# Optimization experiments

Hardware: AMD Instinct MI355X
Metric: run time of the kernel (lower is better)

The kernel has to match this reference:

```python
import jax, jax.numpy as jnp
import numpy as np

B, N, P, L = 32, 4096, 256, 16
DR = 128           # rel_dim = args.rgcn_hidden_size
H = 128            # rnn_hidden_size (unidirectional -> rnn_opt_dim == H)
D = H
NUM_REL = 400      # num_rels * 2


def setup_inputs() -> dict:
    key = jax.random.key(0)
    ks = jax.random.split(key, 12)
    s = 0.05
    graph_embed = jax.random.normal(ks[0], (B, N, DR), jnp.float32)
    node_opt = jax.random.normal(ks[1], (B, D), jnp.float32)
    node_idx = jax.random.randint(ks[2], (B, P, L), 0, N)
    rel_idx = jax.random.randint(ks[3], (B, P, L), 0, NUM_REL)
    path_lens = jax.random.randint(ks[4], (B, P), 1, L + 1)  # in [1, L]
    rel_embeds = jax.random.normal(ks[5], (NUM_REL, DR), jnp.float32) * s
    W_ih = jax.random.normal(ks[6], (4 * H, 2 * DR), jnp.float32) * s
    W_hh = jax.random.normal(ks[7], (4 * H, H), jnp.float32) * s
    b_ih = jnp.zeros((4 * H,), jnp.float32)
    b_hh = jnp.zeros((4 * H,), jnp.float32)
    in_proj_w = jax.random.normal(ks[8], (3 * D, D), jnp.float32) * s
    in_proj_b = jnp.zeros((3 * D,), jnp.float32)
    out_proj_w = jax.random.normal(ks[9], (D, D), jnp.float32) * s
    out_proj_b = jnp.zeros((D,), jnp.float32)
    return dict(graph_embed=graph_embed, node_opt=node_opt, rel_embeds=rel_embeds,
                W_ih=W_ih, W_hh=W_hh, b_ih=b_ih, b_hh=b_hh,
                in_proj_w=in_proj_w, in_proj_b=in_proj_b,
                out_proj_w=out_proj_w, out_proj_b=out_proj_b,
                node_idx=node_idx, rel_idx=rel_idx, path_lens=path_lens)


def _forward(graph_embed, node_opt, rel_embeds, W_ih, W_hh, b_ih, b_hh,
             in_proj_w, in_proj_b, out_proj_w, out_proj_b,
             node_idx, rel_idx, path_lens):
    b, n, dr = graph_embed.shape
    p, l = node_idx.shape[1], node_idx.shape[2]
    h = W_hh.shape[1]
    dt = graph_embed.dtype

    t = jnp.arange(l)
    # node embedding valid for steps < len; rel valid for steps < len-1 ('Padr' at last step -> zero rel half)
    node_mask = (t[None, None, :] < path_lens[:, :, None]).astype(dt)[..., None]
    rel_mask = (t[None, None, :] < (path_lens - 1)[:, :, None]).astype(dt)[..., None]

    batch_ix = jnp.arange(b)[:, None, None]
    node_e = graph_embed[batch_ix, node_idx]            # [B,P,L,DR]
    rel_e = rel_embeds[rel_idx]                          # [B,P,L,DR]
    x = jnp.concatenate([node_e * node_mask, rel_e * rel_mask], axis=-1)
    x = x.reshape(b * p, l, 2 * dr)                      # packed path sequences

    bias = b_ih + b_hh

    def step(carry, xt):
        hh, cc = carry
        g = xt @ W_ih.T + hh @ W_hh.T + bias
        i, f, gg, o = jnp.split(g, 4, axis=-1)
        i = jax.nn.sigmoid(i); f = jax.nn.sigmoid(f)
        gg = jnp.tanh(gg); o = jax.nn.sigmoid(o)
        cc = f * cc + i * gg
        hh = o * jnp.tanh(cc)
        return (hh, cc), hh

    h0 = jnp.zeros((b * p, h), dt)
    _, ys = jax.lax.scan(step, (h0, h0), jnp.swapaxes(x, 0, 1))
    ys = jnp.swapaxes(ys, 0, 1).reshape(b, p, l, h)

    # last valid LSTM output per path (== pack_padded_sequence semantics, unidirectional)
    idx = jnp.broadcast_to((path_lens - 1)[:, :, None, None], (b, p, 1, h))
    last = jnp.take_along_axis(ys, idx, axis=2).squeeze(2)   # [B,P,H]

    # single-head MultiheadAttention: query = node_opt, keys/values = path encodings
    Wq, Wk, Wv = jnp.split(in_proj_w, 3, axis=0)
    bq, bk, bv = jnp.split(in_proj_b, 3)
    q = node_opt @ Wq.T + bq                                  # [B,D]
    k = last @ Wk.T + bk                                      # [B,P,D]
    v = last @ Wv.T + bv
    scale = 1.0 / jnp.sqrt(jnp.asarray(q.shape[-1], dt))
    attn = jax.nn.softmax(jnp.einsum('bd,bpd->bp', q, k) * scale, axis=-1)
    ctx = jnp.einsum('bp,bpd->bd', attn, v)
    return ctx @ out_proj_w.T + out_proj_b                    # [B,D]


def reference(graph_embed, node_opt, rel_embeds, W_ih, W_hh, b_ih, b_hh,
              in_proj_w, in_proj_b, out_proj_w, out_proj_b,
              node_idx, rel_idx, path_lens):
    return _forward(graph_embed, node_opt, rel_embeds, W_ih, W_hh, b_ih, b_hh,
                    in_proj_w, in_proj_b, out_proj_w, out_proj_b,
                    node_idx, rel_idx, path_lens)
```

## Files before the change

kernel.cpp:

```cpp
#include <hip/hip_runtime.h>
#include <hip/hip_bf16.h>


#define B_    32
#define N_    4096
#define L_    16
#define DR_   128
#define H_    128
#define G4_   512
#define AST2  264
#define NPATH 8192
#define NPB   32

typedef unsigned short bfraw;
typedef short short8 __attribute__((ext_vector_type(8)));
typedef float f32x4 __attribute__((ext_vector_type(4)));

__device__ int   g_isbf16;
__device__ int   g_isi64;
__device__ __align__(16) bfraw g_Wcat[G4_ * 256];
__device__ float g_relproj[400 * G4_];
__device__ float g_bias[G4_];
__device__ int   g_perm[NPATH];
__device__ float g_last[NPATH * H_];

__device__ __forceinline__ float bfc(bfraw v) {
    return __uint_as_float(((unsigned)v) << 16);
}
__device__ __forceinline__ bfraw f2b(float f) {
    unsigned u = __float_as_uint(f);
    return (bfraw)((u + 0x7FFFu + ((u >> 16) & 1u)) >> 16);
}
__device__ __forceinline__ unsigned pk2(float a, float b) {
    return (unsigned)f2b(a) | ((unsigned)f2b(b) << 16);
}
__device__ __forceinline__ float ld(const void* p, size_t i, int isbf) {
    return isbf ? bfc(((const bfraw*)p)[i]) : ((const float*)p)[i];
}
__device__ __forceinline__ float sigf(float x) { return 1.0f / (1.0f + __expf(-x)); }
__device__ __forceinline__ float tanhfast(float x) { return 2.0f * sigf(2.0f * x) - 1.0f; }

__device__ __forceinline__ float dot128(const float* __restrict__ w,
                                        const float* __restrict__ s) {
    float acc = 0.f;
    #pragma unroll
    for (int i = 0; i < 32; ++i) {
        const float4 wv = *(const float4*)(w + i * 4);
        acc = fmaf(wv.x, s[i*4+0], fmaf(wv.y, s[i*4+1],
              fmaf(wv.z, s[i*4+2], fmaf(wv.w, s[i*4+3], acc))));
    }
    return acc;
}

__global__ __launch_bounds__(512) void k_prep(
    const void* __restrict__ node_opt, const int* __restrict__ node_idx,
    const void* __restrict__ rel_embeds,
    const void* __restrict__ W_ih, const void* __restrict__ W_hh,
    const void* __restrict__ b_ih, const void* __restrict__ b_hh,
    const int* __restrict__ path_lens)
{
    __shared__ float relv[DR_];
    __shared__ int s_big, s_nz, hist[16], cur[16];
    const int tid = threadIdx.x;
    const int blk = blockIdx.x;

    if (tid == 0) { s_big = 0; s_nz = 0; }
    __syncthreads();
    {
        const unsigned short* u = (const unsigned short*)node_opt;
        int big = 0;
        #pragma unroll
        for (int i = 0; i < 4; ++i) {
            const float v = fabsf(bfc(u[tid + i * 512]));
            big |= !(v < 1.0e3f);
        }
        if (big) s_big = 1;
        if (node_idx[2 * tid + 1] != 0) s_nz = 1;
    }
    __syncthreads();
    const int isbf = s_big ? 0 : 1;
    const int i64  = s_nz ? 0 : 1;

    if (blk < 400) {
        const int r = blk;
        if (tid < DR_) relv[tid] = ld(rel_embeds, (size_t)r * DR_ + tid, isbf);
        __syncthreads();
        const int n = tid;
        float s;
        if (isbf) {
            s = 0.f;
            for (int d = 0; d < DR_; ++d)
                s = fmaf(relv[d], bfc(((const bfraw*)W_ih)[(size_t)n * 256 + 128 + d]), s);
        } else {
            s = dot128((const float*)W_ih + (size_t)n * 256 + 128, relv);
        }
        g_relproj[r * G4_ + n] = s;
    } else if (blk < 656) {
        const int idx = (blk - 400) * 512 + tid;
        const int n = idx >> 8, k = idx & 255;
        const float v = (k < H_) ? ld(W_hh, (size_t)n * H_ + k, isbf)
                                 : ld(W_ih, (size_t)n * 256 + (k - H_), isbf);
        g_Wcat[n * 256 + k] = f2b(v);
    } else {
        if (tid == 0) { g_isbf16 = isbf; g_isi64 = i64; }
        g_bias[tid] = ld(b_ih, tid, isbf) + ld(b_hh, tid, isbf);
        if (tid < 16) hist[tid] = 0;
        __syncthreads();
        for (int p = tid; p < NPATH; p += 512) {
            const int len = i64 ? path_lens[2 * p] : path_lens[p];
            atomicAdd(&hist[len - 1], 1);
        }
        __syncthreads();
        if (tid == 0) {
            int off = 0;
            for (int b = 15; b >= 0; --b) { cur[b] = off; off += hist[b]; }
        }
        __syncthreads();
        for (int p = tid; p < NPATH; p += 512) {
            const int len = i64 ? path_lens[2 * p] : path_lens[p];
            const int pos = atomicAdd(&cur[len - 1], 1);
            g_perm[pos] = p;
        }
    }
}

__global__ __launch_bounds__(512, 2) void k_lstm(
    const void* __restrict__ graph_embed,
    const int*  __restrict__ node_idx,
    const int*  __restrict__ rel_idx,
    const int*  __restrict__ path_lens)
{
    __shared__ __align__(16) bfraw A[NPB][AST2];
    __shared__ int s_pid[NPB], s_len[NPB];
    __shared__ int s_nid[NPB][L_], s_rid[NPB][L_];

    const int isbf = g_isbf16;
    const int i64  = g_isi64;
    const int tid  = threadIdx.x;

    if (tid < NPB) {
        const int pid = g_perm[blockIdx.x * NPB + tid];
        s_pid[tid] = pid;
        s_len[tid] = i64 ? path_lens[2 * pid] : path_lens[pid];
    }
    __syncthreads();
    {
        const int m = tid >> 4, t = tid & 15;
        const int idx = s_pid[m] * L_ + t;
        s_nid[m][t] = i64 ? node_idx[2 * idx] : node_idx[idx];
        s_rid[m][t] = i64 ? rel_idx[2 * idx]  : rel_idx[idx];
    }
    {
        const int m = tid >> 4, i0 = (tid & 15) * 8;
        *(uint4*)&A[m][i0] = make_uint4(0, 0, 0, 0);
    }
    __syncthreads();

    int maxlen = 0;
    #pragma unroll
    for (int m = 0; m < NPB; ++m) maxlen = max(maxlen, s_len[m]);

    const int w    = tid >> 6;
    const int l    = tid & 63;
    const int quad = l >> 4;
    const int col  = l & 15;
    const int u0   = w * 16 + col;

    short8 wreg[8][4];
    float bq4[4];
    #pragma unroll
    for (int g = 0; g < 4; ++g) {
        bq4[g] = g_bias[g * 128 + u0];
        const bfraw* wrow = g_Wcat + (size_t)(g * 128 + u0) * 256 + quad * 8;
        #pragma unroll
        for (int ck = 0; ck < 8; ++ck)
            wreg[ck][g] = *(const short8*)(wrow + ck * 32);
    }

    const int pm  = tid >> 4;
    const int pi0 = (tid & 15) * 8;
    const size_t gbase = (size_t)(s_pid[pm] >> 8) * (size_t)(N_ * DR_);
    uint4 pn0, pn1;
    {
        const int nid = s_nid[pm][0];
        if (isbf) {
            pn0 = *(const uint4*)((const bfraw*)graph_embed + gbase + (size_t)nid * DR_ + pi0);
        } else {
            const float* gp = (const float*)graph_embed + gbase + (size_t)nid * DR_ + pi0;
            pn0 = *(const uint4*)gp; pn1 = *(const uint4*)(gp + 4);
        }
    }

    float c[2][4];
    #pragma unroll
    for (int mt = 0; mt < 2; ++mt)
        #pragma unroll
        for (int r = 0; r < 4; ++r) c[mt][r] = 0.f;

    for (int t = 0; t < maxlen; ++t) {
        {
            uint4 npk = make_uint4(0, 0, 0, 0);
            if (t < s_len[pm]) {
                if (isbf) npk = pn0;
                else {
                    const float* a = (const float*)&pn0;
                    const float* b = (const float*)&pn1;
                    npk = make_uint4(pk2(a[0],a[1]), pk2(a[2],a[3]),
                                     pk2(b[0],b[1]), pk2(b[2],b[3]));
                }
            }
            *(uint4*)&A[pm][128 + pi0] = npk;
        }
        __syncthreads();

        if (t + 1 < maxlen) {
            const int nid = s_nid[pm][t + 1];
            if (isbf) {
                pn0 = *(const uint4*)((const bfraw*)graph_embed + gbase + (size_t)nid * DR_ + pi0);
            } else {
                const float* gp = (const float*)graph_embed + gbase + (size_t)nid * DR_ + pi0;
                pn0 = *(const uint4*)gp; pn1 = *(const uint4*)(gp + 4);
            }
        }

        f32x4 acc[2][4];
        #pragma unroll
        for (int mt = 0; mt < 2; ++mt)
            #pragma unroll
            for (int g = 0; g < 4; ++g) {
                const float b = bq4[g];
                acc[mt][g][0] = b; acc[mt][g][1] = b;
                acc[mt][g][2] = b; acc[mt][g][3] = b;
            }
        #pragma unroll
        for (int ck = 0; ck < 8; ++ck) {
            const short8 a0 = *(const short8*)&A[col][ck * 32 + quad * 8];
            const short8 a1 = *(const short8*)&A[16 + col][ck * 32 + quad * 8];
            #pragma unroll
            for (int g = 0; g < 4; ++g) {
                acc[0][g] = __builtin_amdgcn_mfma_f32_16x16x32_bf16(a0, wreg[ck][g], acc[0][g], 0, 0, 0);
                acc[1][g] = __builtin_amdgcn_mfma_f32_16x16x32_bf16(a1, wreg[ck][g], acc[1][g], 0, 0, 0);
            }
        }

        float rl[2][4][4];
        #pragma unroll
        for (int mt = 0; mt < 2; ++mt)
            #pragma unroll
            for (int r = 0; r < 4; ++r) {
                const int m = mt * 16 + quad * 4 + r;
                const float* rp = g_relproj + (size_t)s_rid[m][t] * G4_ + u0;
                #pragma unroll
                for (int g = 0; g < 4; ++g) rl[mt][g][r] = rp[g * 128];
            }
        __syncthreads();

        #pragma unroll
        for (int mt = 0; mt < 2; ++mt)
            #pragma unroll
            for (int r = 0; r < 4; ++r) {
                const int m = mt * 16 + quad * 4 + r;
                const float relm = (t < s_len[m] - 1) ? 1.0f : 0.0f;
                const float ig = sigf(acc[mt][0][r] + relm * rl[mt][0][r]);
                const float fg = sigf(acc[mt][1][r] + relm * rl[mt][1][r]);
                const float gg = tanhfast(acc[mt][2][r] + relm * rl[mt][2][r]);
                const float og = sigf(acc[mt][3][r] + relm * rl[mt][3][r]);
                const float cc = fg * c[mt][r] + ig * gg;
                c[mt][r] = cc;
                const float h = og * tanhfast(cc);
                A[m][u0] = f2b(h);
                if (t == s_len[m] - 1)
                    g_last[(size_t)s_pid[m] * H_ + u0] = h;
            }
    }
}

__global__ __launch_bounds__(256) void k_attn(
    const void* __restrict__ node_opt,
    const void* __restrict__ in_proj_w,
    const void* __restrict__ in_proj_b,
    const void* __restrict__ out_proj_w,
    const void* __restrict__ out_proj_b,
    float* __restrict__ out)
{
    const int isbf = g_isbf16;
    const int b = blockIdx.x, tid = threadIdx.x;
    __shared__ __align__(16) float s_no[128], q[128], qk[128], sv2[2][128], ctx[128];
    __shared__ float logits[256];
    __shared__ float red[12];

    if (tid < 128) s_no[tid] = ld(node_opt, b * 128 + tid, isbf);
    __syncthreads();
    if (tid < 128) {
        float s;
        if (isbf) {
            s = 0.f;
            for (int j = 0; j < 128; ++j)
                s = fmaf(s_no[j], ld(in_proj_w, (size_t)tid * 128 + j, 1), s);
        } else {
            s = dot128((const float*)in_proj_w + (size_t)tid * 128, s_no);
        }
        q[tid] = s + ld(in_proj_b, tid, isbf);
    }
    __syncthreads();
    if (tid < 128) {
        float s = 0.f;
        for (int j = 0; j < 128; ++j)
            s = fmaf(q[j], ld(in_proj_w, (size_t)(128 + j) * 128 + tid, isbf), s);
        qk[tid] = s;
    } else if (tid == 128) {
        float s = 0.f;
        for (int j = 0; j < 128; ++j)
            s = fmaf(q[j], ld(in_proj_b, 128 + j, isbf), s);
        red[10] = s;
    }
    __syncthreads();
    {
        const float* lp = g_last + ((size_t)b * 256 + tid) * H_;
        const float s = dot128(lp, qk);
        logits[tid] = (s + red[10]) * 0.08838834764831845f;
    }
    __syncthreads();
    float v = logits[tid];
    #pragma unroll
    for (int off = 32; off > 0; off >>= 1) v = fmaxf(v, __shfl_xor(v, off, 64));
    if ((tid & 63) == 0) red[tid >> 6] = v;
    __syncthreads();
    if (tid == 0) red[8] = fmaxf(fmaxf(red[0], red[1]), fmaxf(red[2], red[3]));
    __syncthreads();
    const float e = __expf(logits[tid] - red[8]);
    float sum = e;
    #pragma unroll
    for (int off = 32; off > 0; off >>= 1) sum += __shfl_xor(sum, off, 64);
    if ((tid & 63) == 0) red[4 + (tid >> 6)] = sum;
    __syncthreads();
    if (tid == 0) red[9] = red[4] + red[5] + red[6] + red[7];
    __syncthreads();
    logits[tid] = e / red[9];
    __syncthreads();
    {
        const int u = tid & 127, half = tid >> 7;
        float s = 0.f;
        const float* lb = g_last + ((size_t)b * 256 + half * 128) * H_ + u;
        for (int p = 0; p < 128; ++p)
            s = fmaf(logits[half * 128 + p], lb[(size_t)p * H_], s);
        sv2[half][u] = s;
    }
    __syncthreads();
    if (tid < 128) q[tid] = sv2[0][tid] + sv2[1][tid];
    __syncthreads();
    if (tid < 128) {
        float s;
        if (isbf) {
            s = 0.f;
            for (int u = 0; u < 128; ++u)
                s = fmaf(q[u], ld(in_proj_w, (size_t)(256 + tid) * 128 + u, 1), s);
        } else {
            s = dot128((const float*)in_proj_w + (size_t)(256 + tid) * 128, q);
        }
        ctx[tid] = s + ld(in_proj_b, 256 + tid, isbf);
    }
    __syncthreads();
    if (tid < 128) {
        float s;
        if (isbf) {
            s = 0.f;
            for (int d = 0; d < 128; ++d)
                s = fmaf(ctx[d], ld(out_proj_w, (size_t)tid * 128 + d, 1), s);
        } else {
            s = dot128((const float*)out_proj_w + (size_t)tid * 128, ctx);
        }
        out[b * 128 + tid] = s + ld(out_proj_b, tid, isbf);
    }
}

extern "C" void kernel_launch(void* const* d_in, const int* in_sizes, int n_in,
                              void* d_out, int out_size, void* d_ws, size_t ws_size,
                              hipStream_t stream)
{
    const void* graph_embed = d_in[0];
    const void* node_opt    = d_in[1];
    const void* rel_embeds  = d_in[2];
    const void* W_ih        = d_in[3];
    const void* W_hh        = d_in[4];
    const void* b_ih        = d_in[5];
    const void* b_hh        = d_in[6];
    const void* in_proj_w   = d_in[7];
    const void* in_proj_b   = d_in[8];
    const void* out_proj_w  = d_in[9];
    const void* out_proj_b  = d_in[10];
    const int* node_idx  = (const int*)d_in[11];
    const int* rel_idx   = (const int*)d_in[12];
    const int* path_lens = (const int*)d_in[13];
    (void)d_ws; (void)ws_size; (void)in_sizes; (void)n_in; (void)out_size;

    hipLaunchKernelGGL(k_prep, dim3(657), dim3(512), 0, stream,
                       node_opt, node_idx, rel_embeds, W_ih, W_hh, b_ih, b_hh,
                       path_lens);
    hipLaunchKernelGGL(k_lstm, dim3(NPATH / NPB), dim3(512), 0, stream,
                       graph_embed, node_idx, rel_idx, path_lens);
    hipLaunchKernelGGL(k_attn, dim3(B_), dim3(256), 0, stream,
                       node_opt, in_proj_w, in_proj_b, out_proj_w, out_proj_b,
                       (float*)d_out);
}
```

Baseline: 233.5 us.

## Split prep, transpose W_ih for coalesced relproj, precompute query-key in prep

The prep kernel is split in two. The first stage writes a transposed copy of the relation half of W_ih and also computes the per-batch query-key vector and bias term that k_attn used to compute itself. The second stage computes relproj with coalesced reads of the transposed weights instead of strided per-thread row reads. In the LSTM kernel, the relproj gather is hoisted above the MFMA loop so its latency overlaps compute, and launch bounds change from two blocks per CU to one. This adds an extra kernel launch, and the extra registers held across the MFMA loop along with the launch-bounds change may reduce occupancy.

Result: slower. 261.2 us (+11.8%).

```diff
diff --git a/kernel.cpp b/kernel.cpp
--- a/kernel.cpp
+++ b/kernel.cpp
@@ -19,8 +19,11 @@
 __device__ int   g_isbf16;
 __device__ int   g_isi64;
 __device__ __align__(16) bfraw g_Wcat[G4_ * 256];
+__device__ __align__(16) float g_WihT[DR_ * G4_];
 __device__ float g_relproj[400 * G4_];
 __device__ float g_bias[G4_];
+__device__ float g_qk[B_ * H_];
+__device__ float g_qbk[B_];
 __device__ int   g_perm[NPATH];
 __device__ float g_last[NPATH * H_];
 
@@ -52,15 +55,15 @@
     return acc;
 }
 
-__global__ __launch_bounds__(512) void k_prep(
+__global__ __launch_bounds__(512) void k_prep1(
     const void* __restrict__ node_opt, const int* __restrict__ node_idx,
-    const void* __restrict__ rel_embeds,
     const void* __restrict__ W_ih, const void* __restrict__ W_hh,
     const void* __restrict__ b_ih, const void* __restrict__ b_hh,
+    const void* __restrict__ in_proj_w, const void* __restrict__ in_proj_b,
     const int* __restrict__ path_lens)
 {
-    __shared__ float relv[DR_];
     __shared__ int s_big, s_nz, hist[16], cur[16];
+    __shared__ float q[128];
     const int tid = threadIdx.x;
     const int blk = blockIdx.x;
 
@@ -81,27 +84,16 @@
     const int isbf = s_big ? 0 : 1;
     const int i64  = s_nz ? 0 : 1;
 
-    if (blk < 400) {
-        const int r = blk;
-        if (tid < DR_) relv[tid] = ld(rel_embeds, (size_t)r * DR_ + tid, isbf);
-        __syncthreads();
-        const int n = tid;
-        float s;
-        if (isbf) {
-            s = 0.f;
-            for (int d = 0; d < DR_; ++d)
-                s = fmaf(relv[d], bfc(((const bfraw*)W_ih)[(size_t)n * 256 + 128 + d]), s);
-        } else {
-            s = dot128((const float*)W_ih + (size_t)n * 256 + 128, relv);
-        }
-        g_relproj[r * G4_ + n] = s;
-    } else if (blk < 656) {
-        const int idx = (blk - 400) * 512 + tid;
+    if (blk < 128) {
+        const int d = blk, n = tid;
+        g_WihT[d * G4_ + n] = ld(W_ih, (size_t)n * 256 + 128 + d, isbf);
+    } else if (blk < 384) {
+        const int idx = (blk - 128) * 512 + tid;
         const int n = idx >> 8, k = idx & 255;
         const float v = (k < H_) ? ld(W_hh, (size_t)n * H_ + k, isbf)
                                  : ld(W_ih, (size_t)n * 256 + (k - H_), isbf);
         g_Wcat[n * 256 + k] = f2b(v);
-    } else {
+    } else if (blk == 384) {
         if (tid == 0) { g_isbf16 = isbf; g_isi64 = i64; }
         g_bias[tid] = ld(b_ih, tid, isbf) + ld(b_hh, tid, isbf);
         if (tid < 16) hist[tid] = 0;
@@ -121,10 +113,46 @@
             const int pos = atomicAdd(&cur[len - 1], 1);
             g_perm[pos] = p;
         }
-    }
-}
-
-__global__ __launch_bounds__(512, 2) void k_lstm(
+    } else {
+        const int b = blk - 385;
+        if (tid < 128) {
+            float s = 0.f;
+            for (int j = 0; j < 128; ++j)
+                s = fmaf(ld(node_opt, b * 128 + j, isbf),
+                         ld(in_proj_w, (size_t)tid * 128 + j, isbf), s);
+            q[tid] = s + ld(in_proj_b, tid, isbf);
+        }
+        __syncthreads();
+        if (tid < 128) {
+            float s = 0.f;
+            for (int j = 0; j < 128; ++j)
+                s = fmaf(q[j], ld(in_proj_w, (size_t)(128 + j) * 128 + tid, isbf), s);
+            g_qk[b * 128 + tid] = s;
+        } else if (tid == 128) {
+            float s = 0.f;
+            for (int j = 0; j < 128; ++j)
+                s = fmaf(q[j], ld(in_proj_b, 128 + j, isbf), s);
+            g_qbk[b] = s;
+        }
+    }
+}
+
+__global__ __launch_bounds__(512) void k_prep2(const void* __restrict__ rel_embeds)
+{
+    __shared__ float relv[DR_];
+    const int isbf = g_isbf16;
+    const int r = blockIdx.x;
+    const int n = threadIdx.x;
+    if (n < DR_) relv[n] = ld(rel_embeds, (size_t)r * DR_ + n, isbf);
+    __syncthreads();
+    float s = 0.f;
+    #pragma unroll 4
+    for (int d = 0; d < DR_; ++d)
+        s = fmaf(relv[d], g_WihT[d * G4_ + n], s);
+    g_relproj[r * G4_ + n] = s;
+}
+
+__global__ __launch_bounds__(512, 1) void k_lstm(
     const void* __restrict__ graph_embed,
     const int*  __restrict__ node_idx,
     const int*  __restrict__ rel_idx,
@@ -213,6 +241,16 @@
         }
         __syncthreads();
 
+        float rl[2][4][4];
+        #pragma unroll
+        for (int mt = 0; mt < 2; ++mt)
+            #pragma unroll
+            for (int r = 0; r < 4; ++r) {
+                const int m = mt * 16 + quad * 4 + r;
+                const float* rp = g_relproj + (size_t)s_rid[m][t] * G4_ + u0;
+                #pragma unroll
+                for (int g = 0; g < 4; ++g) rl[mt][g][r] = rp[g * 128];
+            }
         if (t + 1 < maxlen) {
             const int nid = s_nid[pm][t + 1];
             if (isbf) {
@@ -242,17 +280,6 @@
                 acc[1][g] = __builtin_amdgcn_mfma_f32_16x16x32_bf16(a1, wreg[ck][g], acc[1][g], 0, 0, 0);
             }
         }
-
-        float rl[2][4][4];
-        #pragma unroll
-        for (int mt = 0; mt < 2; ++mt)
-            #pragma unroll
-            for (int r = 0; r < 4; ++r) {
-                const int m = mt * 16 + quad * 4 + r;
-                const float* rp = g_relproj + (size_t)s_rid[m][t] * G4_ + u0;
-                #pragma unroll
-                for (int g = 0; g < 4; ++g) rl[mt][g][r] = rp[g * 128];
-            }
         __syncthreads();
 
         #pragma unroll
@@ -276,7 +303,6 @@
 }
 
 __global__ __launch_bounds__(256) void k_attn(
-    const void* __restrict__ node_opt,
     const void* __restrict__ in_proj_w,
     const void* __restrict__ in_proj_b,
     const void* __restrict__ out_proj_w,
@@ -285,40 +311,16 @@
 {
     const int isbf = g_isbf16;
     const int b = blockIdx.x, tid = threadIdx.x;
-    __shared__ __align__(16) float s_no[128], q[128], qk[128], sv2[2][128], ctx[128];
+    __shared__ __align__(16) float qk[128], sv2[2][128], ctx[128], sv[128];
     __shared__ float logits[256];
     __shared__ float red[12];
 
-    if (tid < 128) s_no[tid] = ld(node_opt, b * 128 + tid, isbf);
-    __syncthreads();
-    if (tid < 128) {
-        float s;
-        if (isbf) {
-            s = 0.f;
-            for (int j = 0; j < 128; ++j)
-                s = fmaf(s_no[j], ld(in_proj_w, (size_t)tid * 128 + j, 1), s);
-        } else {
-            s = dot128((const float*)in_proj_w + (size_t)tid * 128, s_no);
-        }
-        q[tid] = s + ld(in_proj_b, tid, isbf);
-    }
-    __syncthreads();
-    if (tid < 128) {
-        float s = 0.f;
-        for (int j = 0; j < 128; ++j)
-            s = fmaf(q[j], ld(in_proj_w, (size_t)(128 + j) * 128 + tid, isbf), s);
-        qk[tid] = s;
-    } else if (tid == 128) {
-        float s = 0.f;
-        for (int j = 0; j < 128; ++j)
-            s = fmaf(q[j], ld(in_proj_b, 128 + j, isbf), s);
-        red[10] = s;
-    }
+    if (tid < 128) qk[tid] = g_qk[b * 128 + tid];
     __syncthreads();
     {
         const float* lp = g_last + ((size_t)b * 256 + tid) * H_;
         const float s = dot128(lp, qk);
-        logits[tid] = (s + red[10]) * 0.08838834764831845f;
+        logits[tid] = (s + g_qbk[b]) * 0.08838834764831845f;
     }
     __syncthreads();
     float v = logits[tid];
@@ -347,16 +349,16 @@
         sv2[half][u] = s;
     }
     __syncthreads();
-    if (tid < 128) q[tid] = sv2[0][tid] + sv2[1][tid];
+    if (tid < 128) sv[tid] = sv2[0][tid] + sv2[1][tid];
     __syncthreads();
     if (tid < 128) {
         float s;
         if (isbf) {
             s = 0.f;
             for (int u = 0; u < 128; ++u)
-                s = fmaf(q[u], ld(in_proj_w, (size_t)(256 + tid) * 128 + u, 1), s);
+                s = fmaf(sv[u], ld(in_proj_w, (size_t)(256 + tid) * 128 + u, 1), s);
         } else {
-            s = dot128((const float*)in_proj_w + (size_t)(256 + tid) * 128, q);
+            s = dot128((const float*)in_proj_w + (size_t)(256 + tid) * 128, sv);
         }
         ctx[tid] = s + ld(in_proj_b, 256 + tid, isbf);
     }
@@ -394,12 +396,13 @@
     const int* path_lens = (const int*)d_in[13];
     (void)d_ws; (void)ws_size; (void)in_sizes; (void)n_in; (void)out_size;
 
-    hipLaunchKernelGGL(k_prep, dim3(657), dim3(512), 0, stream,
-                       node_opt, node_idx, rel_embeds, W_ih, W_hh, b_ih, b_hh,
-                       path_lens);
+    hipLaunchKernelGGL(k_prep1, dim3(417), dim3(512), 0, stream,
+                       node_opt, node_idx, W_ih, W_hh, b_ih, b_hh,
+                       in_proj_w, in_proj_b, path_lens);
+    hipLaunchKernelGGL(k_prep2, dim3(400), dim3(512), 0, stream, rel_embeds);
     hipLaunchKernelGGL(k_lstm, dim3(NPATH / NPB), dim3(512), 0, stream,
                        graph_embed, node_idx, rel_idx, path_lens);
     hipLaunchKernelGGL(k_attn, dim3(B_), dim3(256), 0, stream,
-                       node_opt, in_proj_w, in_proj_b, out_proj_w, out_proj_b,
+                       in_proj_w, in_proj_b, out_proj_w, out_proj_b,
                        (float*)d_out);
 }
```
